# Performance work log

Measured on AMD Instinct MI355X. Metric: run time of the kernel, lower is better.

The kernel has to match this reference:

```python
import jax, jax.numpy as jnp
import numpy as np

B, T, C, H = 4, 4096, 1024, 64

def setup_inputs() -> dict:
    key = jax.random.key(0)
    kx, kq, kk, kv = jax.random.split(key, 4)
    x = jax.random.normal(kx, (B, T, C), dtype=jnp.float32)
    scale = 1.0 / np.sqrt(C)
    Wq = jax.random.normal(kq, (C, H), dtype=jnp.float32) * scale
    Wk = jax.random.normal(kk, (C, H), dtype=jnp.float32) * scale
    Wv = jax.random.normal(kv, (C, H), dtype=jnp.float32) * scale
    return {"x": x, "Wq": Wq, "Wk": Wk, "Wv": Wv}

def reference(x, Wq, Wk, Wv):
    Bsz, Tlen, _ = x.shape
    head_size = Wq.shape[1]
    q = x @ Wq  # [B,T,H]
    k = x @ Wk
    v = x @ Wv
    # scores [B,T,T], scaled by sqrt(head_size)
    scores = jnp.einsum('bqh,bkh->bqk', q, k) / jnp.sqrt(jnp.float32(head_size))
    causal = jnp.tril(jnp.ones((Tlen, Tlen), dtype=bool))
    scores = jnp.where(causal, scores, -jnp.inf)
    weights = jax.nn.softmax(scores, axis=-1)
    # dropout p=0.0 -> identity
    return jnp.einsum('bqk,bkh->bqh', weights, v)
```

## Files before the change

kernel.cpp:

```cpp
#include <hip/hip_runtime.h>
#include <hip/hip_bf16.h>

typedef __attribute__((ext_vector_type(8))) short short8;
typedef __attribute__((ext_vector_type(4))) float f32x4;

#define MFMA16(a, b, c) __builtin_amdgcn_mfma_f32_16x16x32_bf16((a), (b), (c), 0, 0, 0)

__device__ inline unsigned short f2bf(float f) {
    union { float f; unsigned int u; } v;
    v.f = f;
    unsigned int u = v.u;
    return (unsigned short)((u + 0x7fffu + ((u >> 16) & 1u)) >> 16);
}

__device__ inline float bf2f(unsigned short u) {
    union { unsigned int u; float f; } v;
    v.u = ((unsigned int)u) << 16;
    return v.f;
}

__device__ inline size_t WF(int n, int c) {
    return ((((size_t)(n >> 4)) * 32 + (c >> 5)) * 64 + ((c >> 3) & 3) * 16 + (n & 15)) * 8 + (c & 7);
}
__device__ inline size_t QKF(int q, int h) {
    return ((((size_t)(q >> 4)) * 2 + (h >> 5)) * 64 + ((h >> 3) & 3) * 16 + (q & 15)) * 8 + (h & 7);
}
__device__ inline size_t VF(int h, int t) {
    return ((((size_t)(h >> 4)) * 128 + (t >> 5)) * 64 + ((t >> 3) & 3) * 16 + (h & 15)) * 8 + (t & 7);
}

__global__ __launch_bounds__(256) void prep_w(const float* __restrict__ Wq,
                                              const float* __restrict__ Wk,
                                              const float* __restrict__ Wv,
                                              unsigned short* __restrict__ Wt) {
    int idx = blockIdx.x * 256 + threadIdx.x;
    if (idx >= 192 * 1024) return;
    int n = idx >> 10;
    int c = idx & 1023;
    const float* W = (n < 64) ? Wq : ((n < 128) ? Wk : Wv);
    float v = W[c * 64 + (n & 63)];
    if (n < 64) v *= 0.125f;
    Wt[WF(n, c)] = f2bf(v);
}

__global__ __launch_bounds__(256, 4) void projt(const float* __restrict__ x,
                                                const unsigned short* __restrict__ Wt,
                                                unsigned short* __restrict__ Qs,
                                                unsigned short* __restrict__ Ks,
                                                unsigned short* __restrict__ Vt) {
    __shared__ __align__(16) float xbuf[2][16 * 128];

    const int tid = threadIdx.x;
    const int w = tid >> 6;
    const int lane = tid & 63;
    const int lr = lane & 15;
    const int lg = lane >> 4;
    const int t0 = blockIdx.x * 16;

    const int srow0 = w * 4 + (lane >> 5);
    const int schunk = lane & 31;

#define LOADSLAB(v, sl)                                                         \
    {                                                                           \
        const uint4* xr = (const uint4*)(x + (size_t)(t0) * 1024 + (sl) * 128); \
        v[0] = xr[(size_t)(srow0) * 256 + schunk];                              \
        v[1] = xr[(size_t)(srow0 + 2) * 256 + schunk];                          \
    }

#define DSWRITE(buf, v)                                                         \
    {                                                                           \
        _Pragma("unroll")                                                       \
        for (int j = 0; j < 2; j++) {                                           \
            int row = srow0 + j * 2;                                            \
            int l = (schunk & ~15) | ((schunk & 15) ^ (row & 15));              \
            *(uint4*)&xbuf[buf][row * 128 + l * 4] = v[j];                      \
        }                                                                       \
    }

    uint4 vc[2], vn[2];
    LOADSLAB(vc, 0);
    DSWRITE(0, vc);
    LOADSLAB(vc, 1);

    f32x4 acc[3];
#pragma unroll
    for (int i = 0; i < 3; i++) acc[i] = (f32x4){0.f, 0.f, 0.f, 0.f};

#pragma unroll
    for (int t = 0; t < 8; ++t) {
        if (t + 2 < 8) LOADSLAB(vn, t + 2);

        asm volatile("s_waitcnt lgkmcnt(0)" ::: "memory");
        __builtin_amdgcn_sched_barrier(0);
        __builtin_amdgcn_s_barrier();
        __builtin_amdgcn_sched_barrier(0);

        if (t + 1 < 8) DSWRITE((t + 1) & 1, vc);

        const float* xb = &xbuf[t & 1][0];
#pragma unroll
        for (int h = 0; h < 4; h++) {
            short8 bfr[3];
#pragma unroll
            for (int nt = 0; nt < 3; nt++)
                bfr[nt] = *(const short8*)(Wt +
                    (((size_t)(w * 3 + nt) * 32 + (t * 4 + h)) * 64 + lane) * 8);
            int cb = h * 8 + lg * 2;
            int l0 = (cb & ~15) | ((cb & 15) ^ lr);
            int l1 = ((cb + 1) & ~15) | (((cb + 1) & 15) ^ lr);
            float4 a0 = *(const float4*)&xb[lr * 128 + l0 * 4];
            float4 a1 = *(const float4*)&xb[lr * 128 + l1 * 4];
            short8 a;
            a[0] = (short)f2bf(a0.x); a[1] = (short)f2bf(a0.y);
            a[2] = (short)f2bf(a0.z); a[3] = (short)f2bf(a0.w);
            a[4] = (short)f2bf(a1.x); a[5] = (short)f2bf(a1.y);
            a[6] = (short)f2bf(a1.z); a[7] = (short)f2bf(a1.w);
#pragma unroll
            for (int nt = 0; nt < 3; nt++) acc[nt] = MFMA16(a, bfr[nt], acc[nt]);
        }

        if (t + 2 < 8) { vc[0] = vn[0]; vc[1] = vn[1]; }
    }

    const int nbase = w * 48;
#pragma unroll
    for (int nt = 0; nt < 3; nt++) {
#pragma unroll
        for (int r = 0; r < 4; r++) {
            int n = nbase + nt * 16 + lr;
            int tq = t0 + lg * 4 + r;
            int b = tq >> 12;
            int qq = tq & 4095;
            unsigned short val = f2bf(acc[nt][r]);
            if (n < 64) {
                Qs[(size_t)b * 262144 + QKF(qq, n)] = val;
            } else if (n < 128) {
                Ks[(size_t)b * 262144 + QKF(qq, n - 64)] = val;
            } else {
                Vt[(size_t)b * 262144 + VF(n - 128, qq)] = val;
            }
        }
    }
}

#define SROW 72

template <int NS>
__global__ __launch_bounds__(64) void attn(const unsigned short* __restrict__ Qs,
                                           const unsigned short* __restrict__ Ks,
                                           const unsigned short* __restrict__ Vt,
                                           float* __restrict__ out,
                                           unsigned short* __restrict__ accP,
                                           float* __restrict__ mP,
                                           float* __restrict__ lP) {
    __shared__ unsigned short pl[32 * SROW];

    const int ntasks = 512 * NS;
    int raw = ntasks - 1 - blockIdx.x;
    int qt_g = raw / NS;
    int c = raw - qt_g * NS;
    int qt = qt_g >> 2;
    int b = qt_g & 3;
    int q0 = qt * 32;

    int lane = threadIdx.x;
    int lr = lane & 15;
    int lg = lane >> 4;

    const unsigned short* Qb = Qs + (size_t)b * 262144;
    const unsigned short* Kb = Ks + (size_t)b * 262144;
    const unsigned short* Vb = Vt + (size_t)b * 262144;

    short8 qf[2][2];
#pragma unroll
    for (int qs = 0; qs < 2; qs++)
#pragma unroll
        for (int kh = 0; kh < 2; kh++)
            qf[qs][kh] = *(const short8*)(Qb +
                (((size_t)((q0 >> 4) + qs) * 2 + kh) * 64 + lane) * 8);

    f32x4 acc[4][2];
#pragma unroll
    for (int i = 0; i < 4; i++)
#pragma unroll
        for (int qs = 0; qs < 2; qs++) acc[i][qs] = (f32x4){0.f, 0.f, 0.f, 0.f};
    float m[2] = {-1e30f, -1e30f};
    float l[2] = {0.f, 0.f};

    int nt = (q0 + 95) >> 6;
    int tb = (c * nt) / NS;
    int te = ((c + 1) * nt) / NS;

    short8 kf[4][2];
    if (tb < te) {
#pragma unroll
        for (int t = 0; t < 4; t++)
#pragma unroll
            for (int half = 0; half < 2; half++)
                kf[t][half] = *(const short8*)(Kb +
                    (((size_t)((tb * 64) >> 4) + t) * 2 + half) * 512 + lane * 8);
    }

    for (int t64 = tb; t64 < te; ++t64) {
        int kv0 = t64 * 64;

        f32x4 s[4][2];
#pragma unroll
        for (int t = 0; t < 4; t++)
#pragma unroll
            for (int qs = 0; qs < 2; qs++) {
                f32x4 z = (f32x4){0.f, 0.f, 0.f, 0.f};
                z = MFMA16(kf[t][0], qf[qs][0], z);
                z = MFMA16(kf[t][1], qf[qs][1], z);
                s[t][qs] = z;
            }

        short8 vf[4][2];
#pragma unroll
        for (int ht = 0; ht < 4; ht++)
#pragma unroll
            for (int half = 0; half < 2; half++)
                vf[ht][half] = *(const short8*)(Vb +
                    (((size_t)ht * 128 + (kv0 >> 5) + half) * 64 + lane) * 8);

        if (t64 + 1 < te) {
            int kvn = (t64 + 1) * 64;
#pragma unroll
            for (int t = 0; t < 4; t++)
#pragma unroll
                for (int half = 0; half < 2; half++)
                    kf[t][half] = *(const short8*)(Kb +
                        (((size_t)(kvn >> 4) + t) * 2 + half) * 512 + lane * 8);
        }

        if (kv0 + 63 > q0) {
#pragma unroll
            for (int t = 0; t < 4; t++)
#pragma unroll
                for (int qs = 0; qs < 2; qs++)
#pragma unroll
                    for (int r = 0; r < 4; r++) {
                        int kv = kv0 + t * 16 + lg * 4 + r;
                        if (kv > q0 + qs * 16 + lr) s[t][qs][r] = -1e30f;
                    }
        }

        float pmax[2] = {-1e30f, -1e30f};
#pragma unroll
        for (int t = 0; t < 4; t++)
#pragma unroll
            for (int qs = 0; qs < 2; qs++)
#pragma unroll
                for (int r = 0; r < 4; r++) pmax[qs] = fmaxf(pmax[qs], s[t][qs][r]);

        int ok = (pmax[0] <= m[0] + 8.0f) && (pmax[1] <= m[1] + 8.0f);
        if (!__all(ok)) {
            float alpha[2];
#pragma unroll
            for (int qs = 0; qs < 2; qs++) {
                float mx = pmax[qs];
                mx = fmaxf(mx, __shfl_xor(mx, 16));
                mx = fmaxf(mx, __shfl_xor(mx, 32));
                float mn = fmaxf(m[qs], mx);
                alpha[qs] = __expf(m[qs] - mn);
                m[qs] = mn;
                l[qs] *= alpha[qs];
            }
            float ar[2][4];
#pragma unroll
            for (int qs = 0; qs < 2; qs++)
#pragma unroll
                for (int r = 0; r < 4; r++) ar[qs][r] = __shfl(alpha[qs], lg * 4 + r);
#pragma unroll
            for (int ht = 0; ht < 4; ht++)
#pragma unroll
                for (int qs = 0; qs < 2; qs++)
#pragma unroll
                    for (int r = 0; r < 4; r++) acc[ht][qs][r] *= ar[qs][r];
        }

#pragma unroll
        for (int t = 0; t < 4; t++)
#pragma unroll
            for (int qs = 0; qs < 2; qs++)
#pragma unroll
                for (int r = 0; r < 4; r++) {
                    float e = __expf(s[t][qs][r] - m[qs]);
                    s[t][qs][r] = e;
                    l[qs] += e;
                }

#pragma unroll
        for (int qs = 0; qs < 2; qs++)
#pragma unroll
            for (int t = 0; t < 4; t++) {
                uint2 uu;
                uu.x = (unsigned)f2bf(s[t][qs][0]) | ((unsigned)f2bf(s[t][qs][1]) << 16);
                uu.y = (unsigned)f2bf(s[t][qs][2]) | ((unsigned)f2bf(s[t][qs][3]) << 16);
                *(uint2*)&pl[(qs * 16 + lr) * SROW + t * 16 + lg * 4] = uu;
            }
        asm volatile("s_waitcnt lgkmcnt(0)" ::: "memory");
        __builtin_amdgcn_sched_barrier(0);
        short8 pa[2][2];
#pragma unroll
        for (int qs = 0; qs < 2; qs++)
#pragma unroll
            for (int half = 0; half < 2; half++)
                pa[qs][half] = *(const short8*)&pl[(qs * 16 + lr) * SROW +
                                                   half * 32 + lg * 8];

#pragma unroll
        for (int ht = 0; ht < 4; ht++)
#pragma unroll
            for (int qs = 0; qs < 2; qs++) {
                acc[ht][qs] = MFMA16(pa[qs][0], vf[ht][0], acc[ht][qs]);
                acc[ht][qs] = MFMA16(pa[qs][1], vf[ht][1], acc[ht][qs]);
            }
    }

    float lt[2];
#pragma unroll
    for (int qs = 0; qs < 2; qs++) {
        float v = l[qs];
        v += __shfl_xor(v, 16);
        v += __shfl_xor(v, 32);
        lt[qs] = v;
    }

    if (NS == 1) {
        float rl[2][4];
#pragma unroll
        for (int qs = 0; qs < 2; qs++)
#pragma unroll
            for (int r = 0; r < 4; r++) rl[qs][r] = 1.0f / __shfl(lt[qs], lg * 4 + r);
#pragma unroll
        for (int ht = 0; ht < 4; ht++)
#pragma unroll
            for (int qs = 0; qs < 2; qs++)
#pragma unroll
                for (int r = 0; r < 4; r++) {
                    size_t o = ((size_t)b * 4096 + q0 + qs * 16 + lg * 4 + r) * 64 +
                               ht * 16 + lr;
                    out[o] = acc[ht][qs][r] * rl[qs][r];
                }
    } else {
        int tidx = qt_g * NS + c;
        unsigned short* ap = accP + (size_t)tidx * 2048;
#pragma unroll
        for (int ht = 0; ht < 4; ht++)
#pragma unroll
            for (int qs = 0; qs < 2; qs++)
#pragma unroll
                for (int r = 0; r < 4; r++)
                    ap[(qs * 16 + lg * 4 + r) * 64 + ht * 16 + lr] =
                        f2bf(acc[ht][qs][r]);
        if (lane < 16) {
#pragma unroll
            for (int qs = 0; qs < 2; qs++) {
                mP[tidx * 32 + qs * 16 + lane] = m[qs];
                lP[tidx * 32 + qs * 16 + lane] = lt[qs];
            }
        }
    }
}

template <int NS>
__global__ __launch_bounds__(256) void combine(const unsigned short* __restrict__ accP,
                                               const float* __restrict__ mP,
                                               const float* __restrict__ lP,
                                               float* __restrict__ out) {
    int g = blockIdx.x * 256 + threadIdx.x;
    int h = g & 63;
    int row = g >> 6;
    int b = row >> 12;
    int t = row & 4095;
    int qt = t >> 5;
    int qr = t & 31;
    int qt_g = qt * 4 + b;

    float mc[NS];
    float M = -1e30f;
#pragma unroll
    for (int c = 0; c < NS; c++) {
        mc[c] = mP[(qt_g * NS + c) * 32 + qr];
        M = fmaxf(M, mc[c]);
    }
    float num = 0.f, den = 0.f;
#pragma unroll
    for (int c = 0; c < NS; c++) {
        float wgt = __expf(mc[c] - M);
        den += wgt * lP[(qt_g * NS + c) * 32 + qr];
        num += wgt * bf2f(accP[(size_t)(qt_g * NS + c) * 2048 + qr * 64 + h]);
    }
    out[g] = num / den;
}

extern "C" void kernel_launch(void* const* d_in, const int* in_sizes, int n_in,
                              void* d_out, int out_size, void* d_ws, size_t ws_size,
                              hipStream_t stream) {
    const float* x  = (const float*)d_in[0];
    const float* Wq = (const float*)d_in[1];
    const float* Wk = (const float*)d_in[2];
    const float* Wv = (const float*)d_in[3];
    float* out = (float*)d_out;

    char* ws = (char*)d_ws;
    unsigned short* Qs = (unsigned short*)(ws);
    unsigned short* Ks = (unsigned short*)(ws + (2u << 20));
    unsigned short* Vt = (unsigned short*)(ws + (4u << 20));
    unsigned short* Wt = (unsigned short*)(ws + (6u << 20));
    unsigned short* accP = (unsigned short*)(ws + (8u << 20));
    float* mP = (float*)(ws + (24u << 20));
    float* lP = (float*)(ws + (24u << 20) + (512u << 10));

    prep_w<<<768, 256, 0, stream>>>(Wq, Wk, Wv, Wt);
    projt<<<1024, 256, 0, stream>>>(x, Wt, Qs, Ks, Vt);

    if (ws_size >= (25u << 20)) {
        attn<4><<<2048, 64, 0, stream>>>(Qs, Ks, Vt, out, accP, mP, lP);
        combine<4><<<4096, 256, 0, stream>>>(accP, mP, lP, out);
    } else {
        attn<1><<<512, 64, 0, stream>>>(Qs, Ks, Vt, out, accP, mP, lP);
    }
}
```

Baseline: 64.19 us.

## Enlarge projection tile to 64 rows per block to reuse weight fragments

The QKV projection kernel now processes 64 token rows per block instead of 16, staging x in 32-column slabs over 32 pipeline steps. Each weight fragment loaded from global memory is reused across four 16-row groups, cutting weight traffic by four and raising MFMA work per barrier. In exchange the grid shrinks from 1024 to 256 blocks, which may underfill the GPU's compute units, and accumulator register use grows fourfold.

```diff
diff --git a/kernel.cpp b/kernel.cpp
--- a/kernel.cpp
+++ b/kernel.cpp
@@ -48,32 +48,32 @@
                                                 unsigned short* __restrict__ Qs,
                                                 unsigned short* __restrict__ Ks,
                                                 unsigned short* __restrict__ Vt) {
-    __shared__ __align__(16) float xbuf[2][16 * 128];
+    __shared__ __align__(16) float xbuf[2][64 * 32];
 
     const int tid = threadIdx.x;
     const int w = tid >> 6;
     const int lane = tid & 63;
     const int lr = lane & 15;
     const int lg = lane >> 4;
-    const int t0 = blockIdx.x * 16;
-
-    const int srow0 = w * 4 + (lane >> 5);
-    const int schunk = lane & 31;
+    const int t0 = blockIdx.x * 64;
+
+    const int sr0 = w * 16 + (lane >> 3);
+    const int sch = lane & 7;
 
 #define LOADSLAB(v, sl)                                                         \
     {                                                                           \
-        const uint4* xr = (const uint4*)(x + (size_t)(t0) * 1024 + (sl) * 128); \
-        v[0] = xr[(size_t)(srow0) * 256 + schunk];                              \
-        v[1] = xr[(size_t)(srow0 + 2) * 256 + schunk];                          \
+        const uint4* xr = (const uint4*)(x + (size_t)(t0) * 1024) + (sl) * 8;   \
+        v[0] = xr[(size_t)(sr0) * 256 + sch];                                   \
+        v[1] = xr[(size_t)(sr0 + 8) * 256 + sch];                               \
     }
 
 #define DSWRITE(buf, v)                                                         \
     {                                                                           \
         _Pragma("unroll")                                                       \
         for (int j = 0; j < 2; j++) {                                           \
-            int row = srow0 + j * 2;                                            \
-            int l = (schunk & ~15) | ((schunk & 15) ^ (row & 15));              \
-            *(uint4*)&xbuf[buf][row * 128 + l * 4] = v[j];                      \
+            int row = sr0 + j * 8;                                              \
+            int l = sch ^ (row & 7);                                            \
+            *(uint4*)&xbuf[buf][row * 32 + l * 4] = v[j];                       \
         }                                                                       \
     }
 
@@ -82,62 +82,69 @@
     DSWRITE(0, vc);
     LOADSLAB(vc, 1);
 
-    f32x4 acc[3];
-#pragma unroll
-    for (int i = 0; i < 3; i++) acc[i] = (f32x4){0.f, 0.f, 0.f, 0.f};
-
-#pragma unroll
-    for (int t = 0; t < 8; ++t) {
-        if (t + 2 < 8) LOADSLAB(vn, t + 2);
+    f32x4 acc[4][3];
+#pragma unroll
+    for (int rg = 0; rg < 4; rg++)
+#pragma unroll
+        for (int i = 0; i < 3; i++) acc[rg][i] = (f32x4){0.f, 0.f, 0.f, 0.f};
+
+#pragma unroll
+    for (int t = 0; t < 32; ++t) {
+        if (t + 2 < 32) LOADSLAB(vn, t + 2);
 
         asm volatile("s_waitcnt lgkmcnt(0)" ::: "memory");
         __builtin_amdgcn_sched_barrier(0);
         __builtin_amdgcn_s_barrier();
         __builtin_amdgcn_sched_barrier(0);
 
-        if (t + 1 < 8) DSWRITE((t + 1) & 1, vc);
+        if (t + 1 < 32) DSWRITE((t + 1) & 1, vc);
 
         const float* xb = &xbuf[t & 1][0];
-#pragma unroll
-        for (int h = 0; h < 4; h++) {
-            short8 bfr[3];
+        short8 bfr[3];
+#pragma unroll
+        for (int nt = 0; nt < 3; nt++)
+            bfr[nt] = *(const short8*)(Wt +
+                (((size_t)(w * 3 + nt) * 32 + t) * 64 + lane) * 8);
+        int cb = lg * 2;
+#pragma unroll
+        for (int rg = 0; rg < 4; rg++) {
+            int row = rg * 16 + lr;
+            int l0 = (cb) ^ (row & 7);
+            int l1 = (cb + 1) ^ (row & 7);
+            float4 a0 = *(const float4*)&xb[row * 32 + l0 * 4];
+            float4 a1 = *(const float4*)&xb[row * 32 + l1 * 4];
+            short8 av;
+            av[0] = (short)f2bf(a0.x); av[1] = (short)f2bf(a0.y);
+            av[2] = (short)f2bf(a0.z); av[3] = (short)f2bf(a0.w);
+            av[4] = (short)f2bf(a1.x); av[5] = (short)f2bf(a1.y);
+            av[6] = (short)f2bf(a1.z); av[7] = (short)f2bf(a1.w);
 #pragma unroll
             for (int nt = 0; nt < 3; nt++)
-                bfr[nt] = *(const short8*)(Wt +
-                    (((size_t)(w * 3 + nt) * 32 + (t * 4 + h)) * 64 + lane) * 8);
-            int cb = h * 8 + lg * 2;
-            int l0 = (cb & ~15) | ((cb & 15) ^ lr);
-            int l1 = ((cb + 1) & ~15) | (((cb + 1) & 15) ^ lr);
-            float4 a0 = *(const float4*)&xb[lr * 128 + l0 * 4];
-            float4 a1 = *(const float4*)&xb[lr * 128 + l1 * 4];
-            short8 a;
-            a[0] = (short)f2bf(a0.x); a[1] = (short)f2bf(a0.y);
-            a[2] = (short)f2bf(a0.z); a[3] = (short)f2bf(a0.w);
-            a[4] = (short)f2bf(a1.x); a[5] = (short)f2bf(a1.y);
-            a[6] = (short)f2bf(a1.z); a[7] = (short)f2bf(a1.w);
-#pragma unroll
-            for (int nt = 0; nt < 3; nt++) acc[nt] = MFMA16(a, bfr[nt], acc[nt]);
-        }
-
-        if (t + 2 < 8) { vc[0] = vn[0]; vc[1] = vn[1]; }
+                acc[rg][nt] = MFMA16(av, bfr[nt], acc[rg][nt]);
+        }
+
+        if (t + 2 < 32) { vc[0] = vn[0]; vc[1] = vn[1]; }
     }
 
     const int nbase = w * 48;
 #pragma unroll
-    for (int nt = 0; nt < 3; nt++) {
-#pragma unroll
-        for (int r = 0; r < 4; r++) {
-            int n = nbase + nt * 16 + lr;
-            int tq = t0 + lg * 4 + r;
-            int b = tq >> 12;
-            int qq = tq & 4095;
-            unsigned short val = f2bf(acc[nt][r]);
-            if (n < 64) {
-                Qs[(size_t)b * 262144 + QKF(qq, n)] = val;
-            } else if (n < 128) {
-                Ks[(size_t)b * 262144 + QKF(qq, n - 64)] = val;
-            } else {
-                Vt[(size_t)b * 262144 + VF(n - 128, qq)] = val;
+    for (int rg = 0; rg < 4; rg++) {
+#pragma unroll
+        for (int nt = 0; nt < 3; nt++) {
+#pragma unroll
+            for (int r = 0; r < 4; r++) {
+                int n = nbase + nt * 16 + lr;
+                int tq = t0 + rg * 16 + lg * 4 + r;
+                int b = tq >> 12;
+                int qq = tq & 4095;
+                unsigned short val = f2bf(acc[rg][nt][r]);
+                if (n < 64) {
+                    Qs[(size_t)b * 262144 + QKF(qq, n)] = val;
+                } else if (n < 128) {
+                    Ks[(size_t)b * 262144 + QKF(qq, n - 64)] = val;
+                } else {
+                    Vt[(size_t)b * 262144 + VF(n - 128, qq)] = val;
+                }
             }
         }
     }
@@ -414,7 +421,7 @@
     float* lP = (float*)(ws + (24u << 20) + (512u << 10));
 
     prep_w<<<768, 256, 0, stream>>>(Wq, Wk, Wv, Wt);
-    projt<<<1024, 256, 0, stream>>>(x, Wt, Qs, Ks, Vt);
+    projt<<<256, 256, 0, stream>>>(x, Wt, Qs, Ks, Vt);
 
     if (ws_size >= (25u << 20)) {
         attn<4><<<2048, 64, 0, stream>>>(Qs, Ks, Vt, out, accP, mP, lP);
```

Result: slower. 103.5 us (+61.2%).
